# Kernel optimization log

Measured on AMD Instinct MI355X. Metric: run time of the kernel, lower is better.

The kernel has to match this reference:

```python
import jax, jax.numpy as jnp
import numpy as np
import math

D = 1024
H = 16
DK = D // H
FF = 4096
EPS = 1e-5

def _layer_norm(x, gamma, beta):
    mu = jnp.mean(x, axis=-1, keepdims=True)
    var = jnp.mean((x - mu) ** 2, axis=-1, keepdims=True)
    return (x - mu) * jax.lax.rsqrt(var + EPS) * gamma + beta

def setup_inputs() -> dict:
    key = jax.random.key(0)
    ks = jax.random.split(key, 12)
    B, S = 2, 2048
    s = 1.0 / math.sqrt(D)
    inp = {
        "x": jax.random.normal(ks[0], (B, S, D), jnp.float32),
        "attn_mask": jnp.zeros((B, S, S), jnp.bool_),  # True = masked
        "Wq": jax.random.normal(ks[1], (D, D), jnp.float32) * s,
        "Wk": jax.random.normal(ks[2], (D, D), jnp.float32) * s,
        "Wv": jax.random.normal(ks[3], (D, D), jnp.float32) * s,
        "Wo": jax.random.normal(ks[4], (D, D), jnp.float32) * s,
        "bo": jnp.zeros((D,), jnp.float32),
        "W1": jax.random.normal(ks[5], (D, FF), jnp.float32) * s,
        "b1": jnp.zeros((FF,), jnp.float32),
        "W2": jax.random.normal(ks[6], (FF, D), jnp.float32) * (1.0 / math.sqrt(FF)),
        "b2": jnp.zeros((D,), jnp.float32),
        "g1": jnp.ones((D,), jnp.float32),
        "be1": jnp.zeros((D,), jnp.float32),
        "g2": jnp.ones((D,), jnp.float32),
        "be2": jnp.zeros((D,), jnp.float32),
    }
    return inp

def reference(x, attn_mask, Wq, Wk, Wv, Wo, bo, W1, b1, W2, b2, g1, be1, g2, be2):
    B, S, _ = x.shape
    # QKV projections (no bias), split heads -> [B, H, S, DK]
    q = (x @ Wq).reshape(B, S, H, DK).transpose(0, 2, 1, 3)
    k = (x @ Wk).reshape(B, S, H, DK).transpose(0, 2, 1, 3)
    v = (x @ Wv).reshape(B, S, H, DK).transpose(0, 2, 1, 3)
    scores = jnp.einsum("bhqd,bhkd->bhqk", q, k) / math.sqrt(DK)
    scores = jnp.where(attn_mask[:, None, :, :], -jnp.inf, scores)
    attn = jax.nn.softmax(scores, axis=-1)
    attn = jnp.where(jnp.isnan(attn), 0.0, attn)  # fully-masked-row cleanup
    out = jnp.einsum("bhqk,bhkd->bhqd", attn, v)
    out = out.transpose(0, 2, 1, 3).reshape(B, S, D)
    out = out @ Wo + bo
    # residual + post-LN
    x1 = _layer_norm(out + x, g1, be1)
    # FFN
    f = jax.nn.relu(x1 @ W1 + b1) @ W2 + b2
    return _layer_norm(f + x1, g2, be2)
```

## Files before the change

kernel.cpp:

```cpp
#include <hip/hip_runtime.h>
#include <math.h>

typedef unsigned short u16;
typedef unsigned char u8;
typedef unsigned int u32;
typedef __attribute__((ext_vector_type(4))) float f32x4;
typedef __attribute__((ext_vector_type(8))) short s16x8;
typedef __attribute__((ext_vector_type(4))) short s16x4;
typedef __attribute__((ext_vector_type(4))) u32 u32x4;
typedef __attribute__((ext_vector_type(2))) u32 u32x2;

__device__ __forceinline__ u16 f2bf(float f) {
  unsigned u = __builtin_bit_cast(unsigned, f);
  u += 0x7fffu + ((u >> 16) & 1u);
  return (u16)(u >> 16);
}

__device__ __forceinline__ u32 cvtpk_bf16(float lo, float hi) {
  u32 r;
  asm("v_cvt_pk_bf16_f32 %0, %1, %2" : "=v"(r) : "v"(lo), "v"(hi));
  return r;
}

__device__ __forceinline__ float max3f(float a, float b, float c) {
  return fmaxf(fmaxf(a, b), c);
}

#define GLDS16(g, l) __builtin_amdgcn_global_load_lds( \
    (const __attribute__((address_space(1))) void*)(g), \
    (__attribute__((address_space(3))) void*)(l), 16, 0, 0)

template <int EPI, int BM>
__global__ __launch_bounds__(256, 2) void gemm_bt(
    const u16* __restrict__ A, const u16* __restrict__ BT, int M, int N, int K,
    const float* __restrict__ bias, const float* __restrict__ resid,
    u16* __restrict__ outB, float* __restrict__ outF) {
  constexpr int MT = BM / 32;
  __shared__ __align__(16) u16 lA[2][BM * 32];
  __shared__ __align__(16) u16 lB[2][128 * 32];
  const int tid = threadIdx.x;
  const int wave = __builtin_amdgcn_readfirstlane(tid >> 6);
  const int lane = tid & 63;
  const int l15 = lane & 15, l4 = lane >> 4;
  const int wr = wave >> 1, wc = wave & 1;
  const int row0 = blockIdx.y * BM, col0 = blockIdx.x * 128;

  f32x4 acc[MT][4] = {};

  auto stage = [&](int bi, int k0) {
#pragma unroll
    for (int c = 0; c < BM / 64; ++c) {
      const int chunk = c * 4 + wave;
      const int idx = chunk * 64 + lane;
      const int r = idx >> 2, cb = (idx & 3) * 8;
      GLDS16(A + (size_t)(row0 + r) * K + k0 + cb, &lA[bi][chunk * 512]);
    }
#pragma unroll
    for (int c = 0; c < 2; ++c) {
      const int chunk = c * 4 + wave;
      const int idx = chunk * 64 + lane;
      const int r = idx >> 2, cb = (idx & 3) * 8;
      GLDS16(BT + (size_t)(col0 + r) * K + k0 + cb, &lB[bi][chunk * 512]);
    }
  };

  stage(0, 0);
  __syncthreads();
  int buf = 0;

  for (int k0 = 0; k0 < K; k0 += 32) {
    if (k0 + 32 < K) stage(buf ^ 1, k0 + 32);
    s16x8 af[MT], bfr[4];
#pragma unroll
    for (int m = 0; m < MT; ++m)
      af[m] = *(const s16x8*)&lA[buf][(wr * (BM / 2) + m * 16 + l15) * 32 + l4 * 8];
#pragma unroll
    for (int n = 0; n < 4; ++n)
      bfr[n] = *(const s16x8*)&lB[buf][(wc * 64 + n * 16 + l15) * 32 + l4 * 8];
#pragma unroll
    for (int m = 0; m < MT; ++m)
#pragma unroll
      for (int n = 0; n < 4; ++n)
        acc[m][n] = __builtin_amdgcn_mfma_f32_16x16x32_bf16(af[m], bfr[n], acc[m][n], 0, 0, 0);
    __syncthreads();
    buf ^= 1;
  }

#pragma unroll
  for (int m = 0; m < MT; ++m) {
    const int rowb = row0 + wr * (BM / 2) + m * 16 + l4 * 4;
#pragma unroll
    for (int n = 0; n < 4; ++n) {
      const int col = col0 + wc * 64 + n * 16 + l15;
#pragma unroll
      for (int j = 0; j < 4; ++j) {
        const int r = rowb + j;
        float v = acc[m][n][j];
        if (EPI == 0) {
          outB[(size_t)r * N + col] = f2bf(v);
        } else if (EPI == 1) {
          v += bias[col];
          outB[(size_t)r * N + col] = f2bf(v > 0.0f ? v : 0.0f);
        } else {
          v += bias[col] + resid[(size_t)r * N + col];
          outF[(size_t)r * N + col] = v;
        }
      }
    }
  }
}

__global__ __launch_bounds__(256) void transpose_f32_bf16(
    const float* __restrict__ in, u16* __restrict__ out, int R, int C) {
  __shared__ float t[32][33];
  const int c0 = blockIdx.x * 32, r0 = blockIdx.y * 32;
  const int tx = threadIdx.x & 31, ty = threadIdx.x >> 5;
#pragma unroll
  for (int i = 0; i < 4; ++i)
    t[ty + i * 8][tx] = in[(size_t)(r0 + ty + i * 8) * C + c0 + tx];
  __syncthreads();
#pragma unroll
  for (int i = 0; i < 4; ++i)
    out[(size_t)(c0 + ty + i * 8) * R + r0 + tx] = f2bf(t[tx][ty + i * 8]);
}

__global__ __launch_bounds__(256) void transpose_bf16_b(
    const u16* __restrict__ in, u16* __restrict__ out, int R, int C, int rstr, int coff) {
  __shared__ u16 t[32][34];
  const int b = blockIdx.z;
  const u16* pi = in + (size_t)b * R * rstr + coff;
  u16* po = out + (size_t)b * R * C;
  const int c0 = blockIdx.x * 32, r0 = blockIdx.y * 32;
  const int tx = threadIdx.x & 31, ty = threadIdx.x >> 5;
#pragma unroll
  for (int i = 0; i < 4; ++i)
    t[ty + i * 8][tx] = pi[(size_t)(r0 + ty + i * 8) * rstr + c0 + tx];
  __syncthreads();
#pragma unroll
  for (int i = 0; i < 4; ++i)
    po[(size_t)(c0 + ty + i * 8) * R + r0 + tx] = t[tx][ty + i * 8];
}

__global__ __launch_bounds__(256) void cvt_f32_bf16(
    const float* __restrict__ in, u16* __restrict__ out, int n4) {
  const int i = blockIdx.x * 256 + threadIdx.x;
  if (i >= n4) return;
  f32x4 v = *(const f32x4*)&in[(size_t)i * 4];
  s16x4 o;
#pragma unroll
  for (int j = 0; j < 4; ++j) o[j] = (short)f2bf(v[j]);
  *(s16x4*)&out[(size_t)i * 4] = o;
}

template <int WB>
__global__ __launch_bounds__(256) void layernorm_k(
    const float* __restrict__ in, const float* __restrict__ gm, const float* __restrict__ bt,
    float* __restrict__ outF, u16* __restrict__ outB) {
  const int row = blockIdx.x;
  const int t = threadIdx.x;
  const float* xr = in + (size_t)row * 1024;
  f32x4 v = *(const f32x4*)&xr[t * 4];
  float s = v[0] + v[1] + v[2] + v[3];
  float s2 = v[0] * v[0] + v[1] * v[1] + v[2] * v[2] + v[3] * v[3];
#pragma unroll
  for (int o = 32; o; o >>= 1) {
    s += __shfl_down(s, o);
    s2 += __shfl_down(s2, o);
  }
  __shared__ float red[8];
  const int lane = t & 63, wv = t >> 6;
  if (lane == 0) { red[wv] = s; red[4 + wv] = s2; }
  __syncthreads();
  s = red[0] + red[1] + red[2] + red[3];
  s2 = red[4] + red[5] + red[6] + red[7];
  const float mu = s * (1.0f / 1024.0f);
  const float var = fmaxf(s2 * (1.0f / 1024.0f) - mu * mu, 0.0f);
  const float rs = rsqrtf(var + 1e-5f);
  f32x4 g4 = *(const f32x4*)&gm[t * 4];
  f32x4 b4 = *(const f32x4*)&bt[t * 4];
  f32x4 ov;
#pragma unroll
  for (int j = 0; j < 4; ++j) ov[j] = (v[j] - mu) * rs * g4[j] + b4[j];
  *(f32x4*)&outF[(size_t)row * 1024 + t * 4] = ov;
  if (WB) {
    s16x4 ob;
#pragma unroll
    for (int j = 0; j < 4; ++j) ob[j] = (short)f2bf(ov[j]);
    *(s16x4*)&outB[(size_t)row * 1024 + t * 4] = ob;
  }
}

__global__ __launch_bounds__(256) void mask_summary(
    const u8* __restrict__ mask, u8* __restrict__ msum) {
  const int kt = blockIdx.x, qt = blockIdx.y, b = blockIdx.z;
  const int tid = threadIdx.x;
  __shared__ int any_flag;
  if (tid == 0) any_flag = 0;
  __syncthreads();
  const u8* base = mask + ((size_t)(b * 2048 + qt * 64 + (tid >> 2))) * 2048 + kt * 64 + (tid & 3) * 16;
  const u32x4 v = *(const u32x4*)base;
  if (v[0] | v[1] | v[2] | v[3]) any_flag = 1;
  __syncthreads();
  if (tid == 0) msum[((size_t)b * 32 + qt) * 32 + kt] = (u8)any_flag;
}

__global__ __launch_bounds__(256) void attn_k(
    const u16* __restrict__ QKV, const u16* __restrict__ VT,
    const u8* __restrict__ mask, const u8* __restrict__ msum, u16* __restrict__ out) {
  const int S = 2048, QSTR = 3072, Dm = 1024;
  const int wgid = blockIdx.x + gridDim.x * blockIdx.y;
  const int xcd = wgid & 7, slot = wgid >> 3;
  const int bh = xcd * 4 + (slot >> 5);
  const int qt = slot & 31;
  const int b = bh >> 4, h = bh & 15;
  const int wave = threadIdx.x >> 6, lane = threadIdx.x & 63;
  const int l15 = lane & 15, l4 = lane >> 4;
  const int q0 = qt * 64 + wave * 16;
  const float CE = 0.125f * 1.44269504f;

  __shared__ __align__(16) u16 lK[2][4096];
  __shared__ __align__(16) u16 lV[2][4096];

  const size_t qoff = (size_t)(b * S + q0 + l15) * QSTR + h * 64;
  const s16x8 qa0 = *(const s16x8*)&QKV[qoff + l4 * 8];
  const s16x8 qa1 = *(const s16x8*)&QKV[qoff + 32 + l4 * 8];

  f32x4 o[4] = {};
  float mr = -1e30f, lr = 0.0f;
  const u8* mb = mask + (size_t)b * S * S;
  const u8* msb = msum + (size_t)(b * 32 + qt) * 32;
  const u16* vbase = VT + (size_t)bh * 64 * S;
  const int bS = b * S;

  auto stage = [&](int bi, int kvv) {
#pragma unroll
    for (int c = 0; c < 2; ++c) {
      const int byt = ((c * 4 + wave) * 64 + lane) * 16;
      const int row = byt >> 7;
      const int cb = (byt & 127) ^ ((row & 7) << 4);
      GLDS16(QKV + (size_t)(bS + kvv + row) * QSTR + 1024 + h * 64 + (cb >> 1),
             &lK[bi][(c * 4 + wave) * 512]);
      GLDS16(vbase + (size_t)row * S + kvv + (cb >> 1),
             &lV[bi][(c * 4 + wave) * 512]);
    }
  };

  stage(0, 0);
  __syncthreads();
  int buf = 0;

  for (int kv = 0; kv < S; kv += 64) {
    if (kv + 64 < S) stage(buf ^ 1, kv + 64);
    const char* kbuf = (const char*)&lK[buf][0];
    const char* vbuf = (const char*)&lV[buf][0];

    f32x4 sc[4];
    __builtin_amdgcn_s_setprio(1);
#pragma unroll
    for (int t = 0; t < 4; ++t) {
      const int row = t * 16 + l15;
      const int sw = (row & 7) << 4;
      const s16x8 kf0 = *(const s16x8*)(kbuf + row * 128 + ((l4 * 16) ^ sw));
      const s16x8 kf1 = *(const s16x8*)(kbuf + row * 128 + ((64 + l4 * 16) ^ sw));
      f32x4 z = {};
      z = __builtin_amdgcn_mfma_f32_16x16x32_bf16(kf0, qa0, z, 0, 0, 0);
      z = __builtin_amdgcn_mfma_f32_16x16x32_bf16(kf1, qa1, z, 0, 0, 0);
      sc[t] = z;
    }
    __builtin_amdgcn_s_setprio(0);
    if (msb[kv >> 6]) {
#pragma unroll
      for (int t = 0; t < 4; ++t) {
        const uchar4 m4 = *(const uchar4*)&mb[(size_t)(q0 + l15) * S + kv + t * 16 + l4 * 4];
        if (m4.x) sc[t][0] = -INFINITY;
        if (m4.y) sc[t][1] = -INFINITY;
        if (m4.z) sc[t][2] = -INFINITY;
        if (m4.w) sc[t][3] = -INFINITY;
      }
    }
    float pm = max3f(sc[0][0], sc[0][1], sc[0][2]);
    pm = max3f(pm, sc[0][3], sc[1][0]);
    pm = max3f(pm, sc[1][1], sc[1][2]);
    pm = max3f(pm, sc[1][3], sc[2][0]);
    pm = max3f(pm, sc[2][1], sc[2][2]);
    pm = max3f(pm, sc[2][3], sc[3][0]);
    pm = max3f(pm, sc[3][1], sc[3][2]);
    pm = fmaxf(pm, sc[3][3]);
    pm = fmaxf(pm, __shfl_xor(pm, 16));
    pm = fmaxf(pm, __shfl_xor(pm, 32));
    if (!__all(pm <= mr + 44.0f)) {
      const float mn = fmaxf(mr, pm);
      const float al = exp2f((mr - mn) * CE);
      mr = mn;
      lr *= al;
#pragma unroll
      for (int n = 0; n < 4; ++n)
#pragma unroll
        for (int j = 0; j < 4; ++j) o[n][j] *= al;
    }
    const float mrc = mr * CE;
    float rsum = 0.0f;
#pragma unroll
    for (int t = 0; t < 4; ++t)
#pragma unroll
      for (int j = 0; j < 4; ++j) {
        const float p = exp2f(fmaf(sc[t][j], CE, -mrc));
        sc[t][j] = p;
        rsum += p;
      }
    rsum += __shfl_xor(rsum, 16);
    rsum += __shfl_xor(rsum, 32);
    lr += rsum;
    s16x4 pb[4];
#pragma unroll
    for (int t = 0; t < 4; ++t) {
      const u32 lo = cvtpk_bf16(sc[t][0], sc[t][1]);
      const u32 hi = cvtpk_bf16(sc[t][2], sc[t][3]);
      pb[t] = __builtin_bit_cast(s16x4, u32x2{lo, hi});
    }
    __builtin_amdgcn_s_setprio(1);
#pragma unroll
    for (int n = 0; n < 4; ++n) {
      const int row = n * 16 + l15;
      const int sw = (row & 7) << 4;
#pragma unroll
      for (int t = 0; t < 4; ++t) {
        const s16x4 va = *(const s16x4*)(vbuf + row * 128 + ((t * 32 + l4 * 8) ^ sw));
        o[n] = __builtin_amdgcn_mfma_f32_16x16x16bf16_1k(va, pb[t], o[n], 0, 0, 0);
      }
    }
    __builtin_amdgcn_s_setprio(0);
    __syncthreads();
    buf ^= 1;
  }
  const float inv = lr > 0.0f ? 1.0f / lr : 0.0f;
  const size_t obase = (size_t)(b * S + q0 + l15) * Dm + h * 64;
#pragma unroll
  for (int n = 0; n < 4; ++n) {
    const u32 lo = cvtpk_bf16(o[n][0] * inv, o[n][1] * inv);
    const u32 hi = cvtpk_bf16(o[n][2] * inv, o[n][3] * inv);
    *(u32x2*)&out[obase + n * 16 + l4 * 4] = u32x2{lo, hi};
  }
}

extern "C" void kernel_launch(void* const* d_in, const int* in_sizes, int n_in,
                              void* d_out, int out_size, void* d_ws, size_t ws_size,
                              hipStream_t stream) {
  (void)in_sizes; (void)n_in; (void)out_size; (void)ws_size;
  const float* x = (const float*)d_in[0];
  const u8* mask = (const u8*)d_in[1];
  const float* Wq = (const float*)d_in[2];
  const float* Wk = (const float*)d_in[3];
  const float* Wv = (const float*)d_in[4];
  const float* Wo = (const float*)d_in[5];
  const float* bo = (const float*)d_in[6];
  const float* W1 = (const float*)d_in[7];
  const float* b1 = (const float*)d_in[8];
  const float* W2 = (const float*)d_in[9];
  const float* b2 = (const float*)d_in[10];
  const float* g1 = (const float*)d_in[11];
  const float* be1 = (const float*)d_in[12];
  const float* g2 = (const float*)d_in[13];
  const float* be2 = (const float*)d_in[14];
  float* outp = (float*)d_out;

  const int B = 2, S = 2048, D = 1024, FF = 4096;
  const int M = B * S;
  char* w = (char*)d_ws;
  const size_t MB = 1024 * 1024;
  u16* wqkvT = (u16*)(w + 0 * MB);
  u16* woT = (u16*)(w + 6 * MB);
  u16* w1T = (u16*)(w + 8 * MB);
  u16* w2T = (u16*)(w + 16 * MB);
  u16* xb  = (u16*)(w + 24 * MB);
  u16* qkv = (u16*)(w + 32 * MB);
  u16* vt  = (u16*)(w + 56 * MB);
  float* x0f = (float*)(w + 64 * MB);
  float* x1f = (float*)(w + 80 * MB);
  u16* x1b = (u16*)(w + 96 * MB);
  u8* msum = (u8*)(w + 64 * MB);
  u16* attn_o = xb;
  u16* ff1 = (u16*)(w + 32 * MB);
  float* y0f = x0f;

  transpose_f32_bf16<<<dim3(32, 32), 256, 0, stream>>>(Wq, wqkvT, 1024, 1024);
  transpose_f32_bf16<<<dim3(32, 32), 256, 0, stream>>>(Wk, wqkvT + 1024 * 1024, 1024, 1024);
  transpose_f32_bf16<<<dim3(32, 32), 256, 0, stream>>>(Wv, wqkvT + 2048 * 1024, 1024, 1024);
  transpose_f32_bf16<<<dim3(32, 32), 256, 0, stream>>>(Wo, woT, 1024, 1024);
  transpose_f32_bf16<<<dim3(128, 32), 256, 0, stream>>>(W1, w1T, 1024, 4096);
  transpose_f32_bf16<<<dim3(32, 128), 256, 0, stream>>>(W2, w2T, 4096, 1024);
  cvt_f32_bf16<<<dim3(M * D / 4 / 256), 256, 0, stream>>>(x, xb, M * D / 4);
  mask_summary<<<dim3(32, 32, 2), 256, 0, stream>>>(mask, msum);

  gemm_bt<0, 128><<<dim3(3 * D / 128, M / 128), 256, 0, stream>>>(xb, wqkvT, M, 3 * D, D, nullptr, nullptr, qkv, nullptr);
  transpose_bf16_b<<<dim3(32, 64, 2), 256, 0, stream>>>(qkv, vt, 2048, 1024, 3072, 2048);

  attn_k<<<dim3(32, 32), 256, 0, stream>>>(qkv, vt, mask, msum, attn_o);

  gemm_bt<2, 64><<<dim3(D / 128, M / 64), 256, 0, stream>>>(attn_o, woT, M, D, D, bo, x, nullptr, x0f);
  layernorm_k<1><<<dim3(M), 256, 0, stream>>>(x0f, g1, be1, x1f, x1b);
  gemm_bt<1, 128><<<dim3(FF / 128, M / 128), 256, 0, stream>>>(x1b, w1T, M, FF, D, b1, nullptr, ff1, nullptr);
  gemm_bt<2, 64><<<dim3(D / 128, M / 64), 256, 0, stream>>>(ff1, w2T, M, D, FF, b2, x1f, nullptr, y0f);
  layernorm_k<0><<<dim3(M), 256, 0, stream>>>(y0f, g2, be2, outp, nullptr);
}
```

Measured before the change: 295.5 us.

## Swizzle GEMM workgroups across XCDs and compute softmax row sums via MFMA

GEMM blocks are remapped so that consecutive tiles land on the same XCD, aiming for better L2 reuse of A/B tiles. In attention, the per-row probability sum is accumulated with an MFMA against a ones vector instead of VALU adds plus cross-lane shuffles. The KV loop is manually unrolled by two so buffer indices are compile-time constants. Masked scores now use -1e30 instead of -inf, and the attention grid becomes 1-D. This trades extra MFMA issue for fewer shuffles, and changes fully-masked-row behaviour slightly.

```diff
diff --git a/kernel.cpp b/kernel.cpp
--- a/kernel.cpp
+++ b/kernel.cpp
@@ -43,7 +43,11 @@
   const int lane = tid & 63;
   const int l15 = lane & 15, l4 = lane >> 4;
   const int wr = wave >> 1, wc = wave & 1;
-  const int row0 = blockIdx.y * BM, col0 = blockIdx.x * 128;
+  const int nwg = gridDim.x * gridDim.y;
+  int wg = blockIdx.y * gridDim.x + blockIdx.x;
+  wg = (wg & 7) * (nwg >> 3) + (wg >> 3);
+  const int bx = wg % gridDim.x, by = wg / gridDim.x;
+  const int row0 = by * BM, col0 = bx * 128;
 
   f32x4 acc[MT][4] = {};
 
@@ -208,7 +212,7 @@
     const u16* __restrict__ QKV, const u16* __restrict__ VT,
     const u8* __restrict__ mask, const u8* __restrict__ msum, u16* __restrict__ out) {
   const int S = 2048, QSTR = 3072, Dm = 1024;
-  const int wgid = blockIdx.x + gridDim.x * blockIdx.y;
+  const int wgid = blockIdx.x;
   const int xcd = wgid & 7, slot = wgid >> 3;
   const int bh = xcd * 4 + (slot >> 5);
   const int qt = slot & 31;
@@ -217,6 +221,7 @@
   const int l15 = lane & 15, l4 = lane >> 4;
   const int q0 = qt * 64 + wave * 16;
   const float CE = 0.125f * 1.44269504f;
+  const s16x4 ones = {(short)0x3F80, (short)0x3F80, (short)0x3F80, (short)0x3F80};
 
   __shared__ __align__(16) u16 lK[2][4096];
   __shared__ __align__(16) u16 lV[2][4096];
@@ -226,7 +231,8 @@
   const s16x8 qa1 = *(const s16x8*)&QKV[qoff + 32 + l4 * 8];
 
   f32x4 o[4] = {};
-  float mr = -1e30f, lr = 0.0f;
+  f32x4 lacc = {};
+  float mr = -1e30f;
   const u8* mb = mask + (size_t)b * S * S;
   const u8* msb = msum + (size_t)(b * 32 + qt) * 32;
   const u16* vbase = VT + (size_t)bh * 64 * S;
@@ -245,14 +251,10 @@
     }
   };
 
-  stage(0, 0);
-  __syncthreads();
-  int buf = 0;
-
-  for (int kv = 0; kv < S; kv += 64) {
-    if (kv + 64 < S) stage(buf ^ 1, kv + 64);
-    const char* kbuf = (const char*)&lK[buf][0];
-    const char* vbuf = (const char*)&lV[buf][0];
+  auto body = [&](int bi, int kvv) {
+    if (kvv + 64 < S) stage(bi ^ 1, kvv + 64);
+    const char* kbuf = (const char*)&lK[bi][0];
+    const char* vbuf = (const char*)&lV[bi][0];
 
     f32x4 sc[4];
     __builtin_amdgcn_s_setprio(1);
@@ -268,14 +270,14 @@
       sc[t] = z;
     }
     __builtin_amdgcn_s_setprio(0);
-    if (msb[kv >> 6]) {
+    if (msb[kvv >> 6]) {
 #pragma unroll
       for (int t = 0; t < 4; ++t) {
-        const uchar4 m4 = *(const uchar4*)&mb[(size_t)(q0 + l15) * S + kv + t * 16 + l4 * 4];
-        if (m4.x) sc[t][0] = -INFINITY;
-        if (m4.y) sc[t][1] = -INFINITY;
-        if (m4.z) sc[t][2] = -INFINITY;
-        if (m4.w) sc[t][3] = -INFINITY;
+        const uchar4 m4 = *(const uchar4*)&mb[(size_t)(q0 + l15) * S + kvv + t * 16 + l4 * 4];
+        if (m4.x) sc[t][0] = -1e30f;
+        if (m4.y) sc[t][1] = -1e30f;
+        if (m4.z) sc[t][2] = -1e30f;
+        if (m4.w) sc[t][3] = -1e30f;
       }
     }
     float pm = max3f(sc[0][0], sc[0][1], sc[0][2]);
@@ -292,25 +294,19 @@
       const float mn = fmaxf(mr, pm);
       const float al = exp2f((mr - mn) * CE);
       mr = mn;
-      lr *= al;
+#pragma unroll
+      for (int j = 0; j < 4; ++j) lacc[j] *= al;
 #pragma unroll
       for (int n = 0; n < 4; ++n)
 #pragma unroll
         for (int j = 0; j < 4; ++j) o[n][j] *= al;
     }
     const float mrc = mr * CE;
-    float rsum = 0.0f;
 #pragma unroll
     for (int t = 0; t < 4; ++t)
 #pragma unroll
-      for (int j = 0; j < 4; ++j) {
-        const float p = exp2f(fmaf(sc[t][j], CE, -mrc));
-        sc[t][j] = p;
-        rsum += p;
-      }
-    rsum += __shfl_xor(rsum, 16);
-    rsum += __shfl_xor(rsum, 32);
-    lr += rsum;
+      for (int j = 0; j < 4; ++j)
+        sc[t][j] = exp2f(fmaf(sc[t][j], CE, -mrc));
     s16x4 pb[4];
 #pragma unroll
     for (int t = 0; t < 4; ++t) {
@@ -320,6 +316,9 @@
     }
     __builtin_amdgcn_s_setprio(1);
 #pragma unroll
+    for (int t = 0; t < 4; ++t)
+      lacc = __builtin_amdgcn_mfma_f32_16x16x16bf16_1k(ones, pb[t], lacc, 0, 0, 0);
+#pragma unroll
     for (int n = 0; n < 4; ++n) {
       const int row = n * 16 + l15;
       const int sw = (row & 7) << 4;
@@ -331,9 +330,16 @@
     }
     __builtin_amdgcn_s_setprio(0);
     __syncthreads();
-    buf ^= 1;
-  }
-  const float inv = lr > 0.0f ? 1.0f / lr : 0.0f;
+  };
+
+  stage(0, 0);
+  __syncthreads();
+  for (int kv = 0; kv < S; kv += 128) {
+    body(0, kv);
+    body(1, kv + 64);
+  }
+  const float lsum = lacc[0];
+  const float inv = lsum > 0.0f ? 1.0f / lsum : 0.0f;
   const size_t obase = (size_t)(b * S + q0 + l15) * Dm + h * 64;
 #pragma unroll
   for (int n = 0; n < 4; ++n) {
@@ -395,7 +401,7 @@
   gemm_bt<0, 128><<<dim3(3 * D / 128, M / 128), 256, 0, stream>>>(xb, wqkvT, M, 3 * D, D, nullptr, nullptr, qkv, nullptr);
   transpose_bf16_b<<<dim3(32, 64, 2), 256, 0, stream>>>(qkv, vt, 2048, 1024, 3072, 2048);
 
-  attn_k<<<dim3(32, 32), 256, 0, stream>>>(qkv, vt, mask, msum, attn_o);
+  attn_k<<<dim3(1024), 256, 0, stream>>>(qkv, vt, mask, msum, attn_o);
 
   gemm_bt<2, 64><<<dim3(D / 128, M / 64), 256, 0, stream>>>(attn_o, woT, M, D, D, bo, x, nullptr, x0f);
   layernorm_k<1><<<dim3(M), 256, 0, stream>>>(x0f, g1, be1, x1f, x1b);
```

Measured after the change: 299.5 us. Within noise of the previous version (+1.3%).
